# Performance work log

Hardware: AMD Instinct MI355X
Metric: run time of the kernel (lower is better)

The kernel has to match this reference:

```python
import jax, jax.numpy as jnp
import numpy as np

NU, NI = 100000, 100000   # num users / items
DU, DI = 128, 128         # input feature dims
H, O = 256, 256           # hidden_channels, out_channels
ER, EA = 500000, 500000   # edges: reviews, also_bought


def setup_inputs() -> dict:
    key = jax.random.key(0)
    ks = jax.random.split(key, 30)

    def W(k, i, o):
        return jax.random.normal(k, (i, o), jnp.float32) * np.float32(1.0 / np.sqrt(i))

    return {
        "x_user": jax.random.normal(ks[0], (NU, DU), jnp.float32),
        "x_item": jax.random.normal(ks[1], (NI, DI), jnp.float32),
        "src_rev": jax.random.randint(ks[2], (ER,), 0, NU, jnp.int32),
        "dst_rev": jax.random.randint(ks[3], (ER,), 0, NI, jnp.int32),
        "src_ab": jax.random.randint(ks[4], (EA,), 0, NI, jnp.int32),
        "dst_ab": jax.random.randint(ks[5], (EA,), 0, NI, jnp.int32),
        # layer 1 (SAGEConv per edge type): lin_l (neighbor), lin_r (root), bias on lin_l
        "Wl1_rev": W(ks[6], DU, H), "Wr1_rev": W(ks[7], DI, H), "b1_rev": jnp.zeros((H,), jnp.float32),
        "Wl1_rrev": W(ks[8], DI, H), "Wr1_rrev": W(ks[9], DU, H), "b1_rrev": jnp.zeros((H,), jnp.float32),
        "Wl1_ab": W(ks[10], DI, H), "Wr1_ab": W(ks[11], DI, H), "b1_ab": jnp.zeros((H,), jnp.float32),
        # layer 2
        "Wl2_rev": W(ks[12], H, O), "Wr2_rev": W(ks[13], H, O), "b2_rev": jnp.zeros((O,), jnp.float32),
        "Wl2_rrev": W(ks[14], H, O), "Wr2_rrev": W(ks[15], H, O), "b2_rrev": jnp.zeros((O,), jnp.float32),
        "Wl2_ab": W(ks[16], H, O), "Wr2_ab": W(ks[17], H, O), "b2_ab": jnp.zeros((O,), jnp.float32),
    }


def sage_conv(x_src, x_dst, src, dst, Wl, b, Wr):
    """PyG SAGEConv: lin_l(mean of neighbor feats) + lin_r(x_dst); mean of empty set = 0."""
    n_dst = x_dst.shape[0]
    msg_sum = jax.ops.segment_sum(x_src[src], dst, num_segments=n_dst)   # [n_dst, d_src]
    cnt = jax.ops.segment_sum(jnp.ones(dst.shape, x_src.dtype), dst, num_segments=n_dst)
    mean = msg_sum / jnp.maximum(cnt, 1.0)[:, None]
    return mean @ Wl + b + x_dst @ Wr


def reference(x_user, x_item, src_rev, dst_rev, src_ab, dst_ab,
              Wl1_rev, Wr1_rev, b1_rev, Wl1_rrev, Wr1_rrev, b1_rrev, Wl1_ab, Wr1_ab, b1_ab,
              Wl2_rev, Wr2_rev, b2_rev, Wl2_rrev, Wr2_rrev, b2_rrev, Wl2_ab, Wr2_ab, b2_ab):
    # layer 1 + HeteroConv sum aggregation across edge types per dst node type
    h_item = (sage_conv(x_user, x_item, src_rev, dst_rev, Wl1_rev, b1_rev, Wr1_rev)
              + sage_conv(x_item, x_item, src_ab, dst_ab, Wl1_ab, b1_ab, Wr1_ab))
    # rev_reviews = transpose of reviews: item -> user
    h_user = sage_conv(x_item, x_user, dst_rev, src_rev, Wl1_rrev, b1_rrev, Wr1_rrev)
    h_item = jax.nn.relu(h_item)
    h_user = jax.nn.relu(h_user)
    # layer 2
    o_item = (sage_conv(h_user, h_item, src_rev, dst_rev, Wl2_rev, b2_rev, Wr2_rev)
              + sage_conv(h_item, h_item, src_ab, dst_ab, Wl2_ab, b2_ab, Wr2_ab))
    o_user = sage_conv(h_item, h_user, dst_rev, src_rev, Wl2_rrev, b2_rrev, Wr2_rrev)
    return (o_user, o_item)
```

## Files before the change

### kernel.cpp

```cpp
#include <hip/hip_runtime.h>
#include <hip/hip_bf16.h>

#define NN    100000
#define MPAD  100096
#define ER_   500000
#define EA_   500000
#define F_RELU 2

typedef __attribute__((ext_vector_type(8))) _Float16 f16x8;
typedef __attribute__((ext_vector_type(4))) float f32x4;
typedef __attribute__((address_space(3))) uint lds_uint;
typedef const __attribute__((address_space(1))) uint g_uint;

union H8 { uint4 u; _Float16 h[8]; };
union H1 { _Float16 h; ushort u; };

__device__ __forceinline__ ushort f2h(float f) { H1 c; c.h = (_Float16)f; return c.u; }

__global__ void count_deg(const int* __restrict__ dst, int n_edges, int* __restrict__ cnt) {
    int i = blockIdx.x * blockDim.x + threadIdx.x;
    if (i < n_edges) atomicAdd(&cnt[dst[i]], 1);
}

__global__ void fill_csr(const int* __restrict__ dst, const int* __restrict__ src, int n_edges,
                         const int* __restrict__ ptr, int* __restrict__ cur, int* __restrict__ col) {
    int i = blockIdx.x * blockDim.x + threadIdx.x;
    if (i < n_edges) {
        int d = dst[i];
        int slot = ptr[d] + atomicAdd(&cur[d], 1);
        col[slot] = src[i];
    }
}

__global__ void exscan3(const int* __restrict__ c0, int* __restrict__ p0,
                        const int* __restrict__ c1, int* __restrict__ p1,
                        const int* __restrict__ c2, int* __restrict__ p2, int n) {
    const int* cnt = (blockIdx.x == 0) ? c0 : (blockIdx.x == 1) ? c1 : c2;
    int*       ptr = (blockIdx.x == 0) ? p0 : (blockIdx.x == 1) ? p1 : p2;
    __shared__ int wsum[16];
    __shared__ int s_carry, s_tot;
    int tid = threadIdx.x, lane = tid & 63, wid = tid >> 6;
    if (tid == 0) s_carry = 0;
    __syncthreads();
    for (int base = 0; base < n; base += 4096) {
        int i0 = base + tid * 4;
        int4 v = {0, 0, 0, 0};
        if (i0 + 3 < n) v = *(const int4*)(cnt + i0);
        else {
            if (i0     < n) v.x = cnt[i0];
            if (i0 + 1 < n) v.y = cnt[i0 + 1];
            if (i0 + 2 < n) v.z = cnt[i0 + 2];
        }
        int s = v.x + v.y + v.z + v.w;
        int isc = s;
        #pragma unroll
        for (int off = 1; off < 64; off <<= 1) {
            int t = __shfl_up(isc, off, 64);
            if (lane >= off) isc += t;
        }
        if (lane == 63) wsum[wid] = isc;
        __syncthreads();
        if (wid == 0) {
            int w = (lane < 16) ? wsum[lane] : 0;
            int wsc = w;
            #pragma unroll
            for (int off = 1; off < 16; off <<= 1) {
                int t = __shfl_up(wsc, off, 64);
                if (lane >= off) wsc += t;
            }
            if (lane < 16) wsum[lane] = wsc - w;
            if (lane == 15) s_tot = wsc;
        }
        __syncthreads();
        int excl = s_carry + wsum[wid] + (isc - s);
        if (i0     < n) ptr[i0]     = excl;
        if (i0 + 1 < n) ptr[i0 + 1] = excl + v.x;
        if (i0 + 2 < n) ptr[i0 + 2] = excl + v.x + v.y;
        if (i0 + 3 < n) ptr[i0 + 3] = excl + v.x + v.y + v.z;
        __syncthreads();
        if (tid == 0) s_carry += s_tot;
        __syncthreads();
    }
    if (tid == 0) ptr[n] = s_carry;
}

__global__ void wprep(const float* __restrict__ W0, const float* __restrict__ W1, int K,
                      ushort* __restrict__ T) {
    int i = blockIdx.x * blockDim.x + threadIdx.x;
    if (i >= K * 256) return;
    int k = i >> 8, n = i & 255;
    float v = W0[i];
    if (W1) v += W1[i];
    T[n * K + k] = f2h(v);
}

__global__ void cvt_x(const float* __restrict__ x, ushort* __restrict__ o,
                      long nvalid, long ntotal) {
    long i = ((long)blockIdx.x * blockDim.x + threadIdx.x) * 8;
    if (i >= ntotal) return;
    float4 v0 = {0.f,0.f,0.f,0.f}, v1 = {0.f,0.f,0.f,0.f};
    if (i < nvalid) { v0 = *(const float4*)(x + i); v1 = *(const float4*)(x + i + 4); }
    H8 r;
    r.h[0]=(_Float16)v0.x; r.h[1]=(_Float16)v0.y; r.h[2]=(_Float16)v0.z; r.h[3]=(_Float16)v0.w;
    r.h[4]=(_Float16)v1.x; r.h[5]=(_Float16)v1.y; r.h[6]=(_Float16)v1.z; r.h[7]=(_Float16)v1.w;
    *(uint4*)(o + i) = r.u;
}

__global__ void agg128_h(const ushort* __restrict__ x, const int* __restrict__ ptr,
                         const int* __restrict__ col, ushort* __restrict__ out) {
    int g = blockIdx.x * blockDim.x + threadIdx.x;
    int node = g >> 4, l = g & 15;
    if (node >= MPAD) return;
    size_t ob = (size_t)node * 128 + l * 8;
    if (node >= NN) { *(uint4*)(out + ob) = make_uint4(0,0,0,0); return; }
    int p0 = ptr[node], p1 = ptr[node + 1];
    float a[8] = {0.f,0.f,0.f,0.f,0.f,0.f,0.f,0.f};
    for (int e = p0; e < p1; ++e) {
        H8 v; v.u = *(const uint4*)(x + (size_t)col[e] * 128 + l * 8);
        #pragma unroll
        for (int k = 0; k < 8; k++) a[k] += (float)v.h[k];
    }
    float inv = (p1 > p0) ? 1.0f / (float)(p1 - p0) : 0.0f;
    H8 r;
    #pragma unroll
    for (int k = 0; k < 8; k++) r.h[k] = (_Float16)(a[k] * inv);
    *(uint4*)(out + ob) = r.u;
}

__global__ void agg256_h(const ushort* __restrict__ x, const int* __restrict__ ptr,
                         const int* __restrict__ col, ushort* __restrict__ out) {
    int g = blockIdx.x * blockDim.x + threadIdx.x;
    int node = g >> 5, l = g & 31;
    if (node >= MPAD) return;
    size_t ob = (size_t)node * 256 + l * 8;
    if (node >= NN) { *(uint4*)(out + ob) = make_uint4(0,0,0,0); return; }
    int p0 = ptr[node], p1 = ptr[node + 1];
    float a[8] = {0.f,0.f,0.f,0.f,0.f,0.f,0.f,0.f};
    for (int e = p0; e < p1; ++e) {
        H8 v; v.u = *(const uint4*)(x + (size_t)col[e] * 256 + l * 8);
        #pragma unroll
        for (int k = 0; k < 8; k++) a[k] += (float)v.h[k];
    }
    float inv = (p1 > p0) ? 1.0f / (float)(p1 - p0) : 0.0f;
    H8 r;
    #pragma unroll
    for (int k = 0; k < 8; k++) r.h[k] = (_Float16)(a[k] * inv);
    *(uint4*)(out + ob) = r.u;
}

struct GP {
    const ushort *A0, *W0, *A1, *W1, *A2, *W2;
    int ksh0, ksh1, ksh2;
    int c1, c2, S;
};

__global__ __launch_bounds__(256)
void gemm_f16(GP P, const float* __restrict__ b0, const float* __restrict__ b1,
              float* __restrict__ Cf, ushort* __restrict__ Ch, int flags) {
    __shared__ ushort sA[128 * 64];
    __shared__ ushort sW[128 * 64];
    const int tid = threadIdx.x;
    const int m0 = blockIdx.x * 128, n0 = blockIdx.y * 128;
    const int lane = tid & 63, w = tid >> 6;
    const int wr = (w >> 1) * 64, wc = (w & 1) * 64;
    const int fcol = lane & 15, fq = lane >> 4;
    const int srow = tid >> 3, sc = tid & 7;

    f32x4 acc[4][4];
    #pragma unroll
    for (int i = 0; i < 4; i++)
        #pragma unroll
        for (int j = 0; j < 4; j++) acc[i][j] = (f32x4){0.f,0.f,0.f,0.f};

    #pragma unroll 1
    for (int t = 0; t < P.S; ++t) {
        int p = (t >= P.c1) + (t >= P.c2);
        const ushort* A = (p == 2) ? P.A2 : (p == 1) ? P.A1 : P.A0;
        const ushort* W = (p == 2) ? P.W2 : (p == 1) ? P.W1 : P.W0;
        int ksh = (p == 2) ? P.ksh2 : (p == 1) ? P.ksh1 : P.ksh0;
        int base = (p == 2) ? P.c2 : (p == 1) ? P.c1 : 0;
        int k0 = (t - base) << 6;

        #pragma unroll
        for (int ii = 0; ii < 4; ++ii) {
            int row = ii * 32 + srow;
            int q = sc ^ (row & 7);
            const ushort* srcA = A + (((size_t)(m0 + row)) << ksh) + k0 + q * 8;
            const ushort* srcW = W + (((size_t)(n0 + row)) << ksh) + k0 + q * 8;
            __builtin_amdgcn_global_load_lds((g_uint*)srcA,
                (lds_uint*)(sA + row * 64 + sc * 8), 16, 0, 0);
            __builtin_amdgcn_global_load_lds((g_uint*)srcW,
                (lds_uint*)(sW + row * 64 + sc * 8), 16, 0, 0);
        }
        __syncthreads();

        #pragma unroll
        for (int kk = 0; kk < 2; ++kk) {
            f16x8 a[4], b[4];
            #pragma unroll
            for (int i = 0; i < 4; ++i) {
                int ra = wr + i * 16 + fcol;
                int s = (fq + kk * 4) ^ (ra & 7);
                a[i] = *(const f16x8*)(sA + ra * 64 + s * 8);
            }
            #pragma unroll
            for (int j = 0; j < 4; ++j) {
                int rw = wc + j * 16 + fcol;
                int s = (fq + kk * 4) ^ (rw & 7);
                b[j] = *(const f16x8*)(sW + rw * 64 + s * 8);
            }
            #pragma unroll
            for (int i = 0; i < 4; ++i)
                #pragma unroll
                for (int j = 0; j < 4; ++j)
                    acc[i][j] = __builtin_amdgcn_mfma_f32_16x16x32_f16(a[i], b[j], acc[i][j], 0, 0, 0);
        }
        __syncthreads();
    }

    const bool relu = flags & F_RELU;
    float bb[4];
    #pragma unroll
    for (int j = 0; j < 4; ++j) {
        int cg = n0 + wc + j * 16 + fcol;
        float v = 0.f;
        if (b0) v += b0[cg];
        if (b1) v += b1[cg];
        bb[j] = v;
    }
    #pragma unroll
    for (int i = 0; i < 4; ++i) {
        #pragma unroll
        for (int r = 0; r < 4; ++r) {
            int gm = m0 + wr + i * 16 + fq * 4 + r;
            if (gm >= NN) continue;
            size_t rowb = (size_t)gm * 256;
            #pragma unroll
            for (int j = 0; j < 4; ++j) {
                size_t idx = rowb + n0 + wc + j * 16 + fcol;
                float v = acc[i][j][r] + bb[j];
                if (relu) v = fmaxf(v, 0.f);
                if (Ch) Ch[idx] = f2h(v);
                else    Cf[idx] = v;
            }
        }
    }
}

extern "C" void kernel_launch(void* const* d_in, const int* in_sizes, int n_in,
                              void* d_out, int out_size, void* d_ws, size_t ws_size,
                              hipStream_t stream) {
    const float* x_user = (const float*)d_in[0];
    const float* x_item = (const float*)d_in[1];
    const int* src_rev  = (const int*)d_in[2];
    const int* dst_rev  = (const int*)d_in[3];
    const int* src_ab   = (const int*)d_in[4];
    const int* dst_ab   = (const int*)d_in[5];
    const float* Wl1_rev  = (const float*)d_in[6];
    const float* Wr1_rev  = (const float*)d_in[7];
    const float* b1_rev   = (const float*)d_in[8];
    const float* Wl1_rrev = (const float*)d_in[9];
    const float* Wr1_rrev = (const float*)d_in[10];
    const float* b1_rrev  = (const float*)d_in[11];
    const float* Wl1_ab   = (const float*)d_in[12];
    const float* Wr1_ab   = (const float*)d_in[13];
    const float* b1_ab    = (const float*)d_in[14];
    const float* Wl2_rev  = (const float*)d_in[15];
    const float* Wr2_rev  = (const float*)d_in[16];
    const float* b2_rev   = (const float*)d_in[17];
    const float* Wl2_rrev = (const float*)d_in[18];
    const float* Wr2_rrev = (const float*)d_in[19];
    const float* b2_rrev  = (const float*)d_in[20];
    const float* Wl2_ab   = (const float*)d_in[21];
    const float* Wr2_ab   = (const float*)d_in[22];
    const float* b2_ab    = (const float*)d_in[23];

    float* o_user = (float*)d_out;
    float* o_item = (float*)d_out + (size_t)NN * 256;

    char* ws = (char*)d_ws;
    size_t off = 0;
    auto alloc = [&](size_t bytes) -> void* {
        void* p = ws + off;
        off += (bytes + 255) & ~(size_t)255;
        return p;
    };
    const size_t P256 = (size_t)MPAD * 256 * 2;
    const size_t P128 = (size_t)MPAD * 128 * 2;
    ushort* xu     = (ushort*)alloc(P128);
    ushort* xi     = (ushort*)alloc(P128);
    ushort* slabA  = (ushort*)alloc(P128);
    ushort* slabB  = (ushort*)alloc(P128);
    ushort* hI     = (ushort*)alloc(P256);
    ushort* hU     = (ushort*)alloc(P256);
    ushort* slab2A = (ushort*)alloc(P256);
    ushort* slab2B = (ushort*)alloc(P256);
    const size_t W1SZ = 128 * 256 * 2, W2SZ = 256 * 256 * 2;
    ushort* wt_l1rev  = (ushort*)alloc(W1SZ);
    ushort* wt_l1ab   = (ushort*)alloc(W1SZ);
    ushort* wt_l1rrev = (ushort*)alloc(W1SZ);
    ushort* wt_r1c    = (ushort*)alloc(W1SZ);
    ushort* wt_r1rrev = (ushort*)alloc(W1SZ);
    ushort* wt_l2rev  = (ushort*)alloc(W2SZ);
    ushort* wt_l2ab   = (ushort*)alloc(W2SZ);
    ushort* wt_l2rrev = (ushort*)alloc(W2SZ);
    ushort* wt_r2c    = (ushort*)alloc(W2SZ);
    ushort* wt_r2rrev = (ushort*)alloc(W2SZ);
    int* ptrA = (int*)alloc((NN + 1) * 4);
    int* ptrB = (int*)alloc((NN + 1) * 4);
    int* ptrC = (int*)alloc((NN + 1) * 4);
    int* colA = (int*)alloc((size_t)ER_ * 4);
    int* colB = (int*)alloc((size_t)EA_ * 4);
    int* colC = (int*)alloc((size_t)ER_ * 4);
    int* curA = (int*)alloc((size_t)3 * NN * 4);
    int* curB = curA + NN;
    int* curC = curA + 2 * NN;

    const int TPB = 256;
    dim3 egrid((ER_ + TPB - 1) / TPB);

    hipMemsetAsync(curA, 0, (size_t)3 * NN * 4, stream);
    count_deg<<<egrid, TPB, 0, stream>>>(dst_rev, ER_, curA);
    count_deg<<<egrid, TPB, 0, stream>>>(dst_ab,  EA_, curB);
    count_deg<<<egrid, TPB, 0, stream>>>(src_rev, ER_, curC);
    exscan3<<<3, 1024, 0, stream>>>(curA, ptrA, curB, ptrB, curC, ptrC, NN);
    hipMemsetAsync(curA, 0, (size_t)3 * NN * 4, stream);
    fill_csr<<<egrid, TPB, 0, stream>>>(dst_rev, src_rev, ER_, ptrA, curA, colA);
    fill_csr<<<egrid, TPB, 0, stream>>>(dst_ab,  src_ab,  EA_, ptrB, curB, colB);
    fill_csr<<<egrid, TPB, 0, stream>>>(src_rev, dst_rev, ER_, ptrC, curC, colC);

    dim3 wg1((128 * 256 + TPB - 1) / TPB), wg2((256 * 256 + TPB - 1) / TPB);
    wprep<<<wg1, TPB, 0, stream>>>(Wl1_rev,  nullptr, 128, wt_l1rev);
    wprep<<<wg1, TPB, 0, stream>>>(Wl1_ab,   nullptr, 128, wt_l1ab);
    wprep<<<wg1, TPB, 0, stream>>>(Wl1_rrev, nullptr, 128, wt_l1rrev);
    wprep<<<wg1, TPB, 0, stream>>>(Wr1_rev,  Wr1_ab,  128, wt_r1c);
    wprep<<<wg1, TPB, 0, stream>>>(Wr1_rrev, nullptr, 128, wt_r1rrev);
    wprep<<<wg2, TPB, 0, stream>>>(Wl2_rev,  nullptr, 256, wt_l2rev);
    wprep<<<wg2, TPB, 0, stream>>>(Wl2_ab,   nullptr, 256, wt_l2ab);
    wprep<<<wg2, TPB, 0, stream>>>(Wl2_rrev, nullptr, 256, wt_l2rrev);
    wprep<<<wg2, TPB, 0, stream>>>(Wr2_rev,  Wr2_ab,  256, wt_r2c);
    wprep<<<wg2, TPB, 0, stream>>>(Wr2_rrev, nullptr, 256, wt_r2rrev);

    long n128v = (long)NN * 128, n128t = (long)MPAD * 128;
    dim3 cxg(n128t / 8 / TPB);
    cvt_x<<<cxg, TPB, 0, stream>>>(x_user, xu, n128v, n128t);
    cvt_x<<<cxg, TPB, 0, stream>>>(x_item, xi, n128v, n128t);

    dim3 a128g((size_t)MPAD * 16 / TPB), a256g((size_t)MPAD * 32 / TPB);
    dim3 ggrid(MPAD / 128, 2);

    auto launch_gemm = [&](const ushort* a0, const ushort* w0, int K0,
                           const ushort* a1, const ushort* w1, int K1,
                           const ushort* a2, const ushort* w2, int K2,
                           const float* bias0, const float* bias1,
                           float* cf, ushort* ch, int flags) {
        GP P;
        P.A0 = a0; P.W0 = w0;
        P.A1 = a1 ? a1 : a0; P.W1 = w1 ? w1 : w0;
        P.A2 = a2 ? a2 : a0; P.W2 = w2 ? w2 : w0;
        P.ksh0 = (K0 == 256) ? 8 : 7;
        P.ksh1 = (K1 == 256) ? 8 : 7;
        P.ksh2 = (K2 == 256) ? 8 : 7;
        P.c1 = K0 >> 6; P.c2 = P.c1 + (K1 >> 6); P.S = P.c2 + (K2 >> 6);
        gemm_f16<<<ggrid, TPB, 0, stream>>>(P, bias0, bias1, cf, ch, flags);
    };

    agg128_h<<<a128g, TPB, 0, stream>>>(xu, ptrA, colA, slabA);
    agg128_h<<<a128g, TPB, 0, stream>>>(xi, ptrB, colB, slabB);
    launch_gemm(slabA, wt_l1rev, 128, slabB, wt_l1ab, 128, xi, wt_r1c, 128,
                b1_rev, b1_ab, nullptr, hI, F_RELU);
    agg128_h<<<a128g, TPB, 0, stream>>>(xi, ptrC, colC, slabA);
    launch_gemm(slabA, wt_l1rrev, 128, xu, wt_r1rrev, 128, nullptr, nullptr, 0,
                b1_rrev, nullptr, nullptr, hU, F_RELU);

    agg256_h<<<a256g, TPB, 0, stream>>>(hU, ptrA, colA, slab2A);
    agg256_h<<<a256g, TPB, 0, stream>>>(hI, ptrB, colB, slab2B);
    launch_gemm(slab2A, wt_l2rev, 256, slab2B, wt_l2ab, 256, hI, wt_r2c, 256,
                b2_rev, b2_ab, o_item, nullptr, 0);
    agg256_h<<<a256g, TPB, 0, stream>>>(hI, ptrC, colC, slab2A);
    launch_gemm(slab2A, wt_l2rrev, 256, hU, wt_r2rrev, 256, nullptr, nullptr, 0,
                b2_rrev, nullptr, o_user, nullptr, 0);
}
```

Measured before the change: 972.6 us.

## Batch CSR build, prep, aggregation and GEMM launches into fewer merged kernels

Merges the per-edge-type count and fill kernels into single launches, replaces the three-block serial scan with a three-phase chunked parallel scan, and folds the weight transposes and feature conversions into one prep kernel. Aggregations for all three edge types now run in one launch per layer, and the two GEMMs per layer share one launch via a z-dimension grid. This cuts launch count and fills the GPU better on small kernels. It costs an extra slab buffer per layer, and each GEMM block now selects its parameters at runtime.

```diff
diff --git a/kernel.cpp b/kernel.cpp
--- a/kernel.cpp
+++ b/kernel.cpp
@@ -5,6 +5,7 @@
 #define MPAD  100096
 #define ER_   500000
 #define EA_   500000
+#define NCH   25
 #define F_RELU 2
 
 typedef __attribute__((ext_vector_type(8))) _Float16 f16x8;
@@ -17,98 +18,135 @@
 
 __device__ __forceinline__ ushort f2h(float f) { H1 c; c.h = (_Float16)f; return c.u; }
 
-__global__ void count_deg(const int* __restrict__ dst, int n_edges, int* __restrict__ cnt) {
+__global__ void count3(const int* __restrict__ dst_rev, const int* __restrict__ dst_ab,
+                       const int* __restrict__ src_rev, int* __restrict__ cnt ) {
     int i = blockIdx.x * blockDim.x + threadIdx.x;
-    if (i < n_edges) atomicAdd(&cnt[dst[i]], 1);
-}
-
-__global__ void fill_csr(const int* __restrict__ dst, const int* __restrict__ src, int n_edges,
-                         const int* __restrict__ ptr, int* __restrict__ cur, int* __restrict__ col) {
+    if (i < ER_)                 atomicAdd(&cnt[dst_rev[i]], 1);
+    else if (i < ER_ + EA_)      atomicAdd(&cnt[NN + dst_ab[i - ER_]], 1);
+    else if (i < ER_ + EA_ + ER_) atomicAdd(&cnt[2 * NN + src_rev[i - ER_ - EA_]], 1);
+}
+
+__global__ void fill3(const int* __restrict__ dst_rev, const int* __restrict__ src_rev,
+                      const int* __restrict__ dst_ab, const int* __restrict__ src_ab,
+                      const int* __restrict__ pA, const int* __restrict__ pB,
+                      const int* __restrict__ pC, int* __restrict__ cur ,
+                      int* __restrict__ colA, int* __restrict__ colB, int* __restrict__ colC) {
     int i = blockIdx.x * blockDim.x + threadIdx.x;
-    if (i < n_edges) {
-        int d = dst[i];
-        int slot = ptr[d] + atomicAdd(&cur[d], 1);
-        col[slot] = src[i];
-    }
-}
-
-__global__ void exscan3(const int* __restrict__ c0, int* __restrict__ p0,
-                        const int* __restrict__ c1, int* __restrict__ p1,
-                        const int* __restrict__ c2, int* __restrict__ p2, int n) {
-    const int* cnt = (blockIdx.x == 0) ? c0 : (blockIdx.x == 1) ? c1 : c2;
-    int*       ptr = (blockIdx.x == 0) ? p0 : (blockIdx.x == 1) ? p1 : p2;
-    __shared__ int wsum[16];
-    __shared__ int s_carry, s_tot;
+    if (i < ER_) {
+        int d = dst_rev[i];
+        colA[pA[d] + atomicAdd(&cur[d], 1)] = src_rev[i];
+    } else if (i < ER_ + EA_) {
+        int e = i - ER_, d = dst_ab[e];
+        colB[pB[d] + atomicAdd(&cur[NN + d], 1)] = src_ab[e];
+    } else if (i < ER_ + EA_ + ER_) {
+        int e = i - ER_ - EA_, d = src_rev[e];
+        colC[pC[d] + atomicAdd(&cur[2 * NN + d], 1)] = dst_rev[e];
+    }
+}
+
+__global__ void scan_part(const int* __restrict__ cnt , int* __restrict__ part) {
+    int b = blockIdx.x, a = b / NCH, c = b % NCH;
+    const int* src = cnt + a * NN;
+    int base = c * 4096 + threadIdx.x * 16;
+    int s = 0;
+    #pragma unroll
+    for (int k = 0; k < 16; k += 4) {
+        int i = base + k;
+        if (i + 3 < NN) { int4 v = *(const int4*)(src + i); s += v.x + v.y + v.z + v.w; }
+        else { for (int j = 0; j < 4; j++) if (i + j < NN) s += src[i + j]; }
+    }
+    __shared__ int ws[4];
+    int lane = threadIdx.x & 63, wid = threadIdx.x >> 6;
+    #pragma unroll
+    for (int o = 32; o > 0; o >>= 1) s += __shfl_down(s, o, 64);
+    if (lane == 0) ws[wid] = s;
+    __syncthreads();
+    if (threadIdx.x == 0) part[b] = ws[0] + ws[1] + ws[2] + ws[3];
+}
+
+__global__ void scan_off(const int* __restrict__ part, int* __restrict__ choff,
+                         int* __restrict__ pA, int* __restrict__ pB, int* __restrict__ pC) {
+    int a = threadIdx.x;
+    if (a < 3) {
+        int acc = 0;
+        for (int c = 0; c < NCH; c++) { choff[a * NCH + c] = acc; acc += part[a * NCH + c]; }
+        int* p = (a == 0) ? pA : (a == 1) ? pB : pC;
+        p[NN] = acc;
+    }
+}
+
+__global__ void scan_apply(const int* __restrict__ cnt, const int* __restrict__ choff,
+                           int* __restrict__ pA, int* __restrict__ pB, int* __restrict__ pC) {
+    int b = blockIdx.x, a = b / NCH, c = b % NCH;
+    const int* src = cnt + a * NN;
+    int* ptr = (a == 0) ? pA : (a == 1) ? pB : pC;
     int tid = threadIdx.x, lane = tid & 63, wid = tid >> 6;
-    if (tid == 0) s_carry = 0;
+    int base = c * 4096 + tid * 16;
+    int v[16], s = 0;
+    #pragma unroll
+    for (int k = 0; k < 16; k++) { int i = base + k; v[k] = (i < NN) ? src[i] : 0; s += v[k]; }
+    int isc = s;
+    #pragma unroll
+    for (int o = 1; o < 64; o <<= 1) { int t = __shfl_up(isc, o, 64); if (lane >= o) isc += t; }
+    __shared__ int wsum[4];
+    if (lane == 63) wsum[wid] = isc;
     __syncthreads();
-    for (int base = 0; base < n; base += 4096) {
-        int i0 = base + tid * 4;
-        int4 v = {0, 0, 0, 0};
-        if (i0 + 3 < n) v = *(const int4*)(cnt + i0);
-        else {
-            if (i0     < n) v.x = cnt[i0];
-            if (i0 + 1 < n) v.y = cnt[i0 + 1];
-            if (i0 + 2 < n) v.z = cnt[i0 + 2];
-        }
-        int s = v.x + v.y + v.z + v.w;
-        int isc = s;
-        #pragma unroll
-        for (int off = 1; off < 64; off <<= 1) {
-            int t = __shfl_up(isc, off, 64);
-            if (lane >= off) isc += t;
-        }
-        if (lane == 63) wsum[wid] = isc;
-        __syncthreads();
-        if (wid == 0) {
-            int w = (lane < 16) ? wsum[lane] : 0;
-            int wsc = w;
-            #pragma unroll
-            for (int off = 1; off < 16; off <<= 1) {
-                int t = __shfl_up(wsc, off, 64);
-                if (lane >= off) wsc += t;
-            }
-            if (lane < 16) wsum[lane] = wsc - w;
-            if (lane == 15) s_tot = wsc;
-        }
-        __syncthreads();
-        int excl = s_carry + wsum[wid] + (isc - s);
-        if (i0     < n) ptr[i0]     = excl;
-        if (i0 + 1 < n) ptr[i0 + 1] = excl + v.x;
-        if (i0 + 2 < n) ptr[i0 + 2] = excl + v.x + v.y;
-        if (i0 + 3 < n) ptr[i0 + 3] = excl + v.x + v.y + v.z;
-        __syncthreads();
-        if (tid == 0) s_carry += s_tot;
-        __syncthreads();
-    }
-    if (tid == 0) ptr[n] = s_carry;
-}
-
-__global__ void wprep(const float* __restrict__ W0, const float* __restrict__ W1, int K,
-                      ushort* __restrict__ T) {
-    int i = blockIdx.x * blockDim.x + threadIdx.x;
-    if (i >= K * 256) return;
-    int k = i >> 8, n = i & 255;
-    float v = W0[i];
-    if (W1) v += W1[i];
-    T[n * K + k] = f2h(v);
-}
-
-__global__ void cvt_x(const float* __restrict__ x, ushort* __restrict__ o,
-                      long nvalid, long ntotal) {
-    long i = ((long)blockIdx.x * blockDim.x + threadIdx.x) * 8;
-    if (i >= ntotal) return;
-    float4 v0 = {0.f,0.f,0.f,0.f}, v1 = {0.f,0.f,0.f,0.f};
-    if (i < nvalid) { v0 = *(const float4*)(x + i); v1 = *(const float4*)(x + i + 4); }
-    H8 r;
-    r.h[0]=(_Float16)v0.x; r.h[1]=(_Float16)v0.y; r.h[2]=(_Float16)v0.z; r.h[3]=(_Float16)v0.w;
-    r.h[4]=(_Float16)v1.x; r.h[5]=(_Float16)v1.y; r.h[6]=(_Float16)v1.z; r.h[7]=(_Float16)v1.w;
-    *(uint4*)(o + i) = r.u;
-}
-
-__global__ void agg128_h(const ushort* __restrict__ x, const int* __restrict__ ptr,
-                         const int* __restrict__ col, ushort* __restrict__ out) {
-    int g = blockIdx.x * blockDim.x + threadIdx.x;
+    int woff = 0;
+    for (int wj = 0; wj < wid; wj++) woff += wsum[wj];
+    int excl = choff[a * NCH + c] + woff + (isc - s);
+    #pragma unroll
+    for (int k = 0; k < 16; k++) { int i = base + k; if (i < NN) ptr[i] = excl; excl += v[k]; }
+}
+
+struct PrepArgs {
+    const float* xsrc[2]; ushort* xdst[2];
+    const float* W0[10]; const float* W1[10]; ushort* T[10];
+};
+
+__global__ void prep_all(PrepArgs A) {
+    const long CVB = (long)MPAD * 128 / 8 / 256;
+    long b = blockIdx.x;
+    if (b < 2 * CVB) {
+        int which = (b >= CVB);
+        long lb = b - which * CVB;
+        long i = (lb * 256 + threadIdx.x) * 8;
+        const float* x = A.xsrc[which];
+        ushort* o = A.xdst[which];
+        float4 v0 = {0.f,0.f,0.f,0.f}, v1 = {0.f,0.f,0.f,0.f};
+        if (i < (long)NN * 128) { v0 = *(const float4*)(x + i); v1 = *(const float4*)(x + i + 4); }
+        H8 r;
+        r.h[0]=(_Float16)v0.x; r.h[1]=(_Float16)v0.y; r.h[2]=(_Float16)v0.z; r.h[3]=(_Float16)v0.w;
+        r.h[4]=(_Float16)v1.x; r.h[5]=(_Float16)v1.y; r.h[6]=(_Float16)v1.z; r.h[7]=(_Float16)v1.w;
+        *(uint4*)(o + i) = r.u;
+        return;
+    }
+    long j = (b - 2 * CVB) * 256 + threadIdx.x;
+    int idx, rem, K;
+    if (j < 5 * 32768) { idx = j >> 15; rem = j & 32767; K = 128; }
+    else {
+        long j2 = j - 5 * 32768;
+        if (j2 >= 5L * 65536) return;
+        idx = 5 + (int)(j2 >> 16); rem = (int)(j2 & 65535); K = 256;
+    }
+    int k = rem >> 8, n = rem & 255;
+    float v = A.W0[idx][rem];
+    if (A.W1[idx]) v += A.W1[idx][rem];
+    A.T[idx][n * K + k] = f2h(v);
+}
+
+__global__ void agg3_128(const ushort* __restrict__ xu, const ushort* __restrict__ xi,
+                         const int* __restrict__ pA, const int* __restrict__ cA,
+                         const int* __restrict__ pB, const int* __restrict__ cB,
+                         const int* __restrict__ pC, const int* __restrict__ cC,
+                         ushort* __restrict__ sA, ushort* __restrict__ sB,
+                         ushort* __restrict__ sC) {
+    const int SEG = MPAD * 16 / 256;
+    int seg = blockIdx.x / SEG, lb = blockIdx.x % SEG;
+    const ushort* x; const int* ptr; const int* col; ushort* out;
+    if (seg == 0)      { x = xu; ptr = pA; col = cA; out = sA; }
+    else if (seg == 1) { x = xi; ptr = pB; col = cB; out = sB; }
+    else               { x = xi; ptr = pC; col = cC; out = sC; }
+    int g = lb * 256 + threadIdx.x;
     int node = g >> 4, l = g & 15;
     if (node >= MPAD) return;
     size_t ob = (size_t)node * 128 + l * 8;
@@ -127,9 +165,19 @@
     *(uint4*)(out + ob) = r.u;
 }
 
-__global__ void agg256_h(const ushort* __restrict__ x, const int* __restrict__ ptr,
-                         const int* __restrict__ col, ushort* __restrict__ out) {
-    int g = blockIdx.x * blockDim.x + threadIdx.x;
+__global__ void agg3_256(const ushort* __restrict__ hU, const ushort* __restrict__ hI,
+                         const int* __restrict__ pA, const int* __restrict__ cA,
+                         const int* __restrict__ pB, const int* __restrict__ cB,
+                         const int* __restrict__ pC, const int* __restrict__ cC,
+                         ushort* __restrict__ sA, ushort* __restrict__ sB,
+                         ushort* __restrict__ sC) {
+    const int SEG = MPAD * 32 / 256;
+    int seg = blockIdx.x / SEG, lb = blockIdx.x % SEG;
+    const ushort* x; const int* ptr; const int* col; ushort* out;
+    if (seg == 0)      { x = hU; ptr = pA; col = cA; out = sA; }
+    else if (seg == 1) { x = hI; ptr = pB; col = cB; out = sB; }
+    else               { x = hI; ptr = pC; col = cC; out = sC; }
+    int g = lb * 256 + threadIdx.x;
     int node = g >> 5, l = g & 31;
     if (node >= MPAD) return;
     size_t ob = (size_t)node * 256 + l * 8;
@@ -155,8 +203,12 @@
 };
 
 __global__ __launch_bounds__(256)
-void gemm_f16(GP P, const float* __restrict__ b0, const float* __restrict__ b1,
-              float* __restrict__ Cf, ushort* __restrict__ Ch, int flags) {
+void gemm2x(GP Pa, const float* b0a, const float* b1a, float* Cfa, ushort* Cha, int fla,
+            GP Pb, const float* b0b, const float* b1b, float* Cfb, ushort* Chb, int flb) {
+    GP P; const float *b0, *b1; float* Cf; ushort* Ch; int flags;
+    if (blockIdx.z == 0) { P = Pa; b0 = b0a; b1 = b1a; Cf = Cfa; Ch = Cha; flags = fla; }
+    else                 { P = Pb; b0 = b0b; b1 = b1b; Cf = Cfb; Ch = Chb; flags = flb; }
+
     __shared__ ushort sA[128 * 64];
     __shared__ ushort sW[128 * 64];
     const int tid = threadIdx.x;
@@ -177,7 +229,7 @@
         int p = (t >= P.c1) + (t >= P.c2);
         const ushort* A = (p == 2) ? P.A2 : (p == 1) ? P.A1 : P.A0;
         const ushort* W = (p == 2) ? P.W2 : (p == 1) ? P.W1 : P.W0;
-        int ksh = (p == 2) ? P.ksh2 : (p == 1) ? P.ksh1 : P.ksh0;
+        int ksh  = (p == 2) ? P.ksh2 : (p == 1) ? P.ksh1 : P.ksh0;
         int base = (p == 2) ? P.c2 : (p == 1) ? P.c1 : 0;
         int k0 = (t - base) << 6;
 
@@ -291,10 +343,12 @@
     ushort* xi     = (ushort*)alloc(P128);
     ushort* slabA  = (ushort*)alloc(P128);
     ushort* slabB  = (ushort*)alloc(P128);
+    ushort* slabC  = (ushort*)alloc(P128);
     ushort* hI     = (ushort*)alloc(P256);
     ushort* hU     = (ushort*)alloc(P256);
-    ushort* slab2A = (ushort*)alloc(P256);
-    ushort* slab2B = (ushort*)alloc(P256);
+    ushort* s2A    = (ushort*)alloc(P256);
+    ushort* s2B    = (ushort*)alloc(P256);
+    ushort* s2C    = (ushort*)alloc(P256);
     const size_t W1SZ = 128 * 256 * 2, W2SZ = 256 * 256 * 2;
     ushort* wt_l1rev  = (ushort*)alloc(W1SZ);
     ushort* wt_l1ab   = (ushort*)alloc(W1SZ);
@@ -312,48 +366,42 @@
     int* colA = (int*)alloc((size_t)ER_ * 4);
     int* colB = (int*)alloc((size_t)EA_ * 4);
     int* colC = (int*)alloc((size_t)ER_ * 4);
-    int* curA = (int*)alloc((size_t)3 * NN * 4);
-    int* curB = curA + NN;
-    int* curC = curA + 2 * NN;
+    int* cnt3 = (int*)alloc((size_t)3 * NN * 4);
+    int* part  = (int*)alloc(3 * NCH * 4);
+    int* choff = (int*)alloc(3 * NCH * 4);
 
     const int TPB = 256;
-    dim3 egrid((ER_ + TPB - 1) / TPB);
-
-    hipMemsetAsync(curA, 0, (size_t)3 * NN * 4, stream);
-    count_deg<<<egrid, TPB, 0, stream>>>(dst_rev, ER_, curA);
-    count_deg<<<egrid, TPB, 0, stream>>>(dst_ab,  EA_, curB);
-    count_deg<<<egrid, TPB, 0, stream>>>(src_rev, ER_, curC);
-    exscan3<<<3, 1024, 0, stream>>>(curA, ptrA, curB, ptrB, curC, ptrC, NN);
-    hipMemsetAsync(curA, 0, (size_t)3 * NN * 4, stream);
-    fill_csr<<<egrid, TPB, 0, stream>>>(dst_rev, src_rev, ER_, ptrA, curA, colA);
-    fill_csr<<<egrid, TPB, 0, stream>>>(dst_ab,  src_ab,  EA_, ptrB, curB, colB);
-    fill_csr<<<egrid, TPB, 0, stream>>>(src_rev, dst_rev, ER_, ptrC, curC, colC);
-
-    dim3 wg1((128 * 256 + TPB - 1) / TPB), wg2((256 * 256 + TPB - 1) / TPB);
-    wprep<<<wg1, TPB, 0, stream>>>(Wl1_rev,  nullptr, 128, wt_l1rev);
-    wprep<<<wg1, TPB, 0, stream>>>(Wl1_ab,   nullptr, 128, wt_l1ab);
-    wprep<<<wg1, TPB, 0, stream>>>(Wl1_rrev, nullptr, 128, wt_l1rrev);
-    wprep<<<wg1, TPB, 0, stream>>>(Wr1_rev,  Wr1_ab,  128, wt_r1c);
-    wprep<<<wg1, TPB, 0, stream>>>(Wr1_rrev, nullptr, 128, wt_r1rrev);
-    wprep<<<wg2, TPB, 0, stream>>>(Wl2_rev,  nullptr, 256, wt_l2rev);
-    wprep<<<wg2, TPB, 0, stream>>>(Wl2_ab,   nullptr, 256, wt_l2ab);
-    wprep<<<wg2, TPB, 0, stream>>>(Wl2_rrev, nullptr, 256, wt_l2rrev);
-    wprep<<<wg2, TPB, 0, stream>>>(Wr2_rev,  Wr2_ab,  256, wt_r2c);
-    wprep<<<wg2, TPB, 0, stream>>>(Wr2_rrev, nullptr, 256, wt_r2rrev);
-
-    long n128v = (long)NN * 128, n128t = (long)MPAD * 128;
-    dim3 cxg(n128t / 8 / TPB);
-    cvt_x<<<cxg, TPB, 0, stream>>>(x_user, xu, n128v, n128t);
-    cvt_x<<<cxg, TPB, 0, stream>>>(x_item, xi, n128v, n128t);
-
-    dim3 a128g((size_t)MPAD * 16 / TPB), a256g((size_t)MPAD * 32 / TPB);
-    dim3 ggrid(MPAD / 128, 2);
-
-    auto launch_gemm = [&](const ushort* a0, const ushort* w0, int K0,
-                           const ushort* a1, const ushort* w1, int K1,
-                           const ushort* a2, const ushort* w2, int K2,
-                           const float* bias0, const float* bias1,
-                           float* cf, ushort* ch, int flags) {
+    const int NE3 = ER_ + EA_ + ER_;
+    dim3 e3grid((NE3 + TPB - 1) / TPB);
+
+    hipMemsetAsync(cnt3, 0, (size_t)3 * NN * 4, stream);
+    count3<<<e3grid, TPB, 0, stream>>>(dst_rev, dst_ab, src_rev, cnt3);
+    scan_part<<<3 * NCH, TPB, 0, stream>>>(cnt3, part);
+    scan_off<<<1, 64, 0, stream>>>(part, choff, ptrA, ptrB, ptrC);
+    scan_apply<<<3 * NCH, TPB, 0, stream>>>(cnt3, choff, ptrA, ptrB, ptrC);
+    hipMemsetAsync(cnt3, 0, (size_t)3 * NN * 4, stream);
+    fill3<<<e3grid, TPB, 0, stream>>>(dst_rev, src_rev, dst_ab, src_ab,
+                                      ptrA, ptrB, ptrC, cnt3, colA, colB, colC);
+
+    PrepArgs PA;
+    PA.xsrc[0] = x_user; PA.xdst[0] = xu;
+    PA.xsrc[1] = x_item; PA.xdst[1] = xi;
+    const float* W0s[10] = {Wl1_rev, Wl1_ab, Wl1_rrev, Wr1_rev, Wr1_rrev,
+                            Wl2_rev, Wl2_ab, Wl2_rrev, Wr2_rev, Wr2_rrev};
+    const float* W1s[10] = {nullptr, nullptr, nullptr, Wr1_ab, nullptr,
+                            nullptr, nullptr, nullptr, Wr2_ab, nullptr};
+    ushort* Ts[10] = {wt_l1rev, wt_l1ab, wt_l1rrev, wt_r1c, wt_r1rrev,
+                      wt_l2rev, wt_l2ab, wt_l2rrev, wt_r2c, wt_r2rrev};
+    for (int i = 0; i < 10; i++) { PA.W0[i] = W0s[i]; PA.W1[i] = W1s[i]; PA.T[i] = Ts[i]; }
+    const long CVB = (long)MPAD * 128 / 8 / 256;
+    const long WPB = (5 * 32768 + 5 * 65536 + 255) / 256;
+    prep_all<<<(int)(2 * CVB + WPB), TPB, 0, stream>>>(PA);
+
+    dim3 ggrid(MPAD / 128, 2, 2);
+
+    auto mkGP = [&](const ushort* a0, const ushort* w0, int K0,
+                    const ushort* a1, const ushort* w1, int K1,
+                    const ushort* a2, const ushort* w2, int K2) {
         GP P;
         P.A0 = a0; P.W0 = w0;
         P.A1 = a1 ? a1 : a0; P.W1 = w1 ? w1 : w0;
@@ -362,22 +410,24 @@
         P.ksh1 = (K1 == 256) ? 8 : 7;
         P.ksh2 = (K2 == 256) ? 8 : 7;
         P.c1 = K0 >> 6; P.c2 = P.c1 + (K1 >> 6); P.S = P.c2 + (K2 >> 6);
-        gemm_f16<<<ggrid, TPB, 0, stream>>>(P, bias0, bias1, cf, ch, flags);
+        return P;
     };
 
-    agg128_h<<<a128g, TPB, 0, stream>>>(xu, ptrA, colA, slabA);
-    agg128_h<<<a128g, TPB, 0, stream>>>(xi, ptrB, colB, slabB);
-    launch_gemm(slabA, wt_l1rev, 128, slabB, wt_l1ab, 128, xi, wt_r1c, 128,
-                b1_rev, b1_ab, nullptr, hI, F_RELU);
-    agg128_h<<<a128g, TPB, 0, stream>>>(xi, ptrC, colC, slabA);
-    launch_gemm(slabA, wt_l1rrev, 128, xu, wt_r1rrev, 128, nullptr, nullptr, 0,
-                b1_rrev, nullptr, nullptr, hU, F_RELU);
-
-    agg256_h<<<a256g, TPB, 0, stream>>>(hU, ptrA, colA, slab2A);
-    agg256_h<<<a256g, TPB, 0, stream>>>(hI, ptrB, colB, slab2B);
-    launch_gemm(slab2A, wt_l2rev, 256, slab2B, wt_l2ab, 256, hI, wt_r2c, 256,
-                b2_rev, b2_ab, o_item, nullptr, 0);
-    agg256_h<<<a256g, TPB, 0, stream>>>(hI, ptrC, colC, slab2A);
-    launch_gemm(slab2A, wt_l2rrev, 256, hU, wt_r2rrev, 256, nullptr, nullptr, 0,
-                b2_rrev, nullptr, o_user, nullptr, 0);
-}
+    agg3_128<<<3 * (MPAD * 16 / 256), TPB, 0, stream>>>(xu, xi, ptrA, colA, ptrB, colB,
+                                                        ptrC, colC, slabA, slabB, slabC);
+    {
+        GP P0 = mkGP(slabA, wt_l1rev, 128, slabB, wt_l1ab, 128, xi, wt_r1c, 128);
+        GP P1 = mkGP(slabC, wt_l1rrev, 128, xu, wt_r1rrev, 128, nullptr, nullptr, 0);
+        gemm2x<<<ggrid, TPB, 0, stream>>>(P0, b1_rev, b1_ab, nullptr, hI, F_RELU,
+                                          P1, b1_rrev, nullptr, nullptr, hU, F_RELU);
+    }
+
+    agg3_256<<<3 * (MPAD * 32 / 256), TPB, 0, stream>>>(hU, hI, ptrA, colA, ptrB, colB,
+                                                        ptrC, colC, s2A, s2B, s2C);
+    {
+        GP P0 = mkGP(s2A, wt_l2rev, 256, s2B, wt_l2ab, 256, hI, wt_r2c, 256);
+        GP P1 = mkGP(s2C, wt_l2rrev, 256, hU, wt_r2rrev, 256, nullptr, nullptr, 0);
+        gemm2x<<<ggrid, TPB, 0, stream>>>(P0, b2_rev, b2_ab, o_item, nullptr, 0,
+                                          P1, b2_rrev, nullptr, o_user, nullptr, 0);
+    }
+}
```

After: 856.5 us. 1.14x faster.
